# Kernel optimization log

Measured on AMD Instinct MI355X. Metric: run time of the kernel, lower is better.

The kernel has to match this reference:

```python
import jax, jax.numpy as jnp
import numpy as np

N, M, K = 8192, 100000, 4096


def setup_inputs() -> dict:
    key = jax.random.key(0)
    k0, k1, k2, k3, k4, k5 = jax.random.split(key, 6)
    origins = jax.random.uniform(k0, (N, 2), dtype=jnp.float32)
    directions = jax.random.uniform(k1, (N, 2), dtype=jnp.float32)
    embeddings = jax.random.uniform(k2, (M, 4), dtype=jnp.float32)
    # Cholesky factors: lower-triangular with strictly positive diagonal
    # (mirrors Encoder.update_parameters: tril + abs(diag)+eps)
    L = jnp.tril(jax.random.uniform(k3, (M, 4, 4), dtype=jnp.float32) * 0.1)
    i4 = jnp.arange(4)
    diag = jnp.abs(L[:, i4, i4]) + 1e-2
    chol = L.at[:, i4, i4].set(diag)
    # labels_embedding in {-1, +1} (Encoder maps 0 -> -1)
    labels = jnp.where(jax.random.randint(k4, (M,), 0, 2) == 0, -1.0, 1.0).astype(jnp.float32)
    idx = jax.random.randint(k5, (K,), 0, M, dtype=jnp.int32)
    return {"origins": origins, "directions": directions, "embeddings": embeddings,
            "chol": chol, "labels": labels, "idx": idx}


def reference(origins, directions, embeddings, chol, labels, idx):
    # Encoder: gather selected gaussians, Sigma = L @ L^T
    mu = embeddings[idx]                                   # [K,4]
    Lsel = chol[idx]                                       # [K,4,4]
    Sigma = jnp.einsum('kij,klj->kil', Lsel, Lsel)         # [K,4,4]
    lab = labels[idx]                                      # [K]
    # Decoder: batched 4x4 inverse + quadratic form + exp + sum + sigmoid
    Sigma_inv = jnp.linalg.inv(Sigma)                      # [K,4,4]
    pos = jnp.concatenate([origins, directions], axis=1)   # [N,4]
    diffs = pos[:, None, :] - mu[None, :, :]               # [N,K,4]
    q = jnp.einsum('nkd,kde,nke->nk', diffs, Sigma_inv, diffs)  # [N,K]
    pdf = lab[None, :] * jnp.exp(-0.5 * q)                 # [N,K]
    prob = jax.nn.sigmoid(jnp.sum(pdf, axis=1))            # [N]
    return prob.reshape(-1, 1)
```

## Files before the change

### kernel.cpp

```cpp
#include <hip/hip_runtime.h>
#include <math.h>

#define K_TOTAL 4096
#define N_RAYS  8192
#define S_CHUNKS 128
#define CHUNK (K_TOTAL / S_CHUNKS)
#define R 4
#define BLOCK 256
#define RAYS_PER_BLOCK (BLOCK * R)
#define NGROUPS (N_RAYS / RAYS_PER_BLOCK)

__global__ __launch_bounds__(256) void precompute_kernel(
    const float* __restrict__ embeddings,
    const float* __restrict__ chol,
    const float* __restrict__ labels,
    const int*   __restrict__ idx,
    float4*      __restrict__ tab)
{
    int k = blockIdx.x * blockDim.x + threadIdx.x;
    if (k >= K_TOTAL) return;
    int i = idx[k];

    const float* Lp = chol + (size_t)i * 16;
    float l00 = Lp[0];
    float l10 = Lp[4],  l11 = Lp[5];
    float l20 = Lp[8],  l21 = Lp[9],  l22 = Lp[10];
    float l30 = Lp[12], l31 = Lp[13], l32 = Lp[14], l33 = Lp[15];

    float u0 = 1.0f / l00, u1 = 1.0f / l11, u2 = 1.0f / l22, u3 = 1.0f / l33;

    float m00 = u0;
    float m10 = -u1 * (l10 * m00);
    float m11 = u1;
    float m20 = -u2 * (l20 * m00 + l21 * m10);
    float m21 = -u2 * (l21 * m11);
    float m22 = u2;
    float m30 = -u3 * (l30 * m00 + l31 * m10 + l32 * m20);
    float m31 = -u3 * (l31 * m11 + l32 * m21);
    float m32 = -u3 * (l32 * m22);
    float m33 = u3;

    const float SC = 0.84932180381996511548f;
    m00 *= SC; m10 *= SC; m11 *= SC; m20 *= SC; m21 *= SC;
    m22 *= SC; m30 *= SC; m31 *= SC; m32 *= SC; m33 *= SC;

    float4 mu = *(const float4*)(embeddings + (size_t)i * 4);
    float b0 = -(m00 * mu.x);
    float b1 = -(m10 * mu.x + m11 * mu.y);
    float b2 = -(m20 * mu.x + m21 * mu.y + m22 * mu.z);
    float b3 = -(m30 * mu.x + m31 * mu.y + m32 * mu.z + m33 * mu.w);

    float lab = labels[i];

    tab[4*k + 0] = make_float4(m00, m10, m11, m20);
    tab[4*k + 1] = make_float4(m21, m22, m30, m31);
    tab[4*k + 2] = make_float4(m32, m33, b0, b1);
    tab[4*k + 3] = make_float4(b2, b3, lab, 0.0f);
}

__global__ __launch_bounds__(256) void main_kernel(
    const float*  __restrict__ origins,
    const float*  __restrict__ directions,
    const float4* __restrict__ tab,
    float*        __restrict__ partial)
{
    int tid  = threadIdx.x;
    int base = blockIdx.x * RAYS_PER_BLOCK + tid;
    int s    = blockIdx.y;

    float p0[R], p1[R], p2[R], p3[R], acc[R];
    #pragma unroll
    for (int r = 0; r < R; ++r) {
        int n = base + r * BLOCK;
        float2 o = ((const float2*)origins)[n];
        float2 d = ((const float2*)directions)[n];
        p0[r] = o.x; p1[r] = o.y; p2[r] = d.x; p3[r] = d.y;
        acc[r] = 0.0f;
    }

    const float4* __restrict__ t = tab + (size_t)s * CHUNK * 4;

    #pragma unroll 4
    for (int k = 0; k < CHUNK; ++k) {
        float4 t0 = t[4*k + 0];
        float4 t1 = t[4*k + 1];
        float4 t2 = t[4*k + 2];
        float4 t3 = t[4*k + 3];
        #pragma unroll
        for (int r = 0; r < R; ++r) {
            float y0 = fmaf(t0.x, p0[r], t2.z);
            float y1 = fmaf(t0.z, p1[r], fmaf(t0.y, p0[r], t2.w));
            float y2 = fmaf(t1.y, p2[r], fmaf(t1.x, p1[r], fmaf(t0.w, p0[r], t3.x)));
            float y3 = fmaf(t2.y, p3[r], fmaf(t2.x, p2[r], fmaf(t1.w, p1[r], fmaf(t1.z, p0[r], t3.y))));
            float sq = y0 * y0;
            sq = fmaf(y1, y1, sq);
            sq = fmaf(y2, y2, sq);
            sq = fmaf(y3, y3, sq);
            acc[r] = fmaf(t3.z, __builtin_amdgcn_exp2f(-sq), acc[r]);
        }
    }

    #pragma unroll
    for (int r = 0; r < R; ++r)
        partial[(size_t)s * N_RAYS + base + r * BLOCK] = acc[r];
}

__global__ __launch_bounds__(256) void finish_kernel(
    const float* __restrict__ partial,
    float*       __restrict__ out)
{
    int n = blockIdx.x * 256 + threadIdx.x;
    float sum = 0.0f;
    #pragma unroll 8
    for (int s = 0; s < S_CHUNKS; ++s)
        sum += partial[(size_t)s * N_RAYS + n];
    const float L2E = 1.44269504088896340736f;
    out[n] = 1.0f / (1.0f + __builtin_amdgcn_exp2f(-sum * L2E));
}

extern "C" void kernel_launch(void* const* d_in, const int* in_sizes, int n_in,
                              void* d_out, int out_size, void* d_ws, size_t ws_size,
                              hipStream_t stream) {
    const float* origins    = (const float*)d_in[0];
    const float* directions = (const float*)d_in[1];
    const float* embeddings = (const float*)d_in[2];
    const float* chol       = (const float*)d_in[3];
    const float* labels     = (const float*)d_in[4];
    const int*   idx        = (const int*)d_in[5];
    float* out = (float*)d_out;

    float4* tab     = (float4*)d_ws;
    float*  partial = (float*)((char*)d_ws + (size_t)K_TOTAL * 4 * sizeof(float4));

    precompute_kernel<<<dim3(K_TOTAL / 256), dim3(256), 0, stream>>>(
        embeddings, chol, labels, idx, tab);

    main_kernel<<<dim3(NGROUPS, S_CHUNKS), dim3(256), 0, stream>>>(
        origins, directions, tab, partial);

    finish_kernel<<<dim3(N_RAYS / 256), dim3(256), 0, stream>>>(partial, out);
}
```

Baseline: 93.19 us.

## Fuse Gaussian precompute into main kernel via shared-memory table

Removes the separate precompute kernel launch. Each block of the main kernel now computes the 32-entry scaled inverse-Cholesky table for its chunk into shared memory, then reads parameters from LDS instead of global memory. Each chunk's table is recomputed by all 8 ray-group blocks, and a __syncthreads is added. The finish kernel is retuned to 64-thread blocks with a deeper unroll, and the main loop unroll is raised to 8.

```diff
diff --git a/kernel.cpp b/kernel.cpp
--- a/kernel.cpp
+++ b/kernel.cpp
@@ -10,63 +10,62 @@
 #define RAYS_PER_BLOCK (BLOCK * R)
 #define NGROUPS (N_RAYS / RAYS_PER_BLOCK)
 
-__global__ __launch_bounds__(256) void precompute_kernel(
+__global__ __launch_bounds__(256) void fused_main_kernel(
+    const float* __restrict__ origins,
+    const float* __restrict__ directions,
     const float* __restrict__ embeddings,
     const float* __restrict__ chol,
     const float* __restrict__ labels,
     const int*   __restrict__ idx,
-    float4*      __restrict__ tab)
+    float*       __restrict__ partial)
 {
-    int k = blockIdx.x * blockDim.x + threadIdx.x;
-    if (k >= K_TOTAL) return;
-    int i = idx[k];
+    __shared__ float4 stab[CHUNK * 4];
 
-    const float* Lp = chol + (size_t)i * 16;
-    float l00 = Lp[0];
-    float l10 = Lp[4],  l11 = Lp[5];
-    float l20 = Lp[8],  l21 = Lp[9],  l22 = Lp[10];
-    float l30 = Lp[12], l31 = Lp[13], l32 = Lp[14], l33 = Lp[15];
+    int tid = threadIdx.x;
+    int s   = blockIdx.y;
 
-    float u0 = 1.0f / l00, u1 = 1.0f / l11, u2 = 1.0f / l22, u3 = 1.0f / l33;
+    if (tid < CHUNK) {
+        int k = s * CHUNK + tid;
+        int i = idx[k];
 
-    float m00 = u0;
-    float m10 = -u1 * (l10 * m00);
-    float m11 = u1;
-    float m20 = -u2 * (l20 * m00 + l21 * m10);
-    float m21 = -u2 * (l21 * m11);
-    float m22 = u2;
-    float m30 = -u3 * (l30 * m00 + l31 * m10 + l32 * m20);
-    float m31 = -u3 * (l31 * m11 + l32 * m21);
-    float m32 = -u3 * (l32 * m22);
-    float m33 = u3;
+        const float* Lp = chol + (size_t)i * 16;
+        float l00 = Lp[0];
+        float l10 = Lp[4],  l11 = Lp[5];
+        float l20 = Lp[8],  l21 = Lp[9],  l22 = Lp[10];
+        float l30 = Lp[12], l31 = Lp[13], l32 = Lp[14], l33 = Lp[15];
 
-    const float SC = 0.84932180381996511548f;
-    m00 *= SC; m10 *= SC; m11 *= SC; m20 *= SC; m21 *= SC;
-    m22 *= SC; m30 *= SC; m31 *= SC; m32 *= SC; m33 *= SC;
+        float u0 = 1.0f / l00, u1 = 1.0f / l11, u2 = 1.0f / l22, u3 = 1.0f / l33;
 
-    float4 mu = *(const float4*)(embeddings + (size_t)i * 4);
-    float b0 = -(m00 * mu.x);
-    float b1 = -(m10 * mu.x + m11 * mu.y);
-    float b2 = -(m20 * mu.x + m21 * mu.y + m22 * mu.z);
-    float b3 = -(m30 * mu.x + m31 * mu.y + m32 * mu.z + m33 * mu.w);
+        float m00 = u0;
+        float m10 = -u1 * (l10 * m00);
+        float m11 = u1;
+        float m20 = -u2 * (l20 * m00 + l21 * m10);
+        float m21 = -u2 * (l21 * m11);
+        float m22 = u2;
+        float m30 = -u3 * (l30 * m00 + l31 * m10 + l32 * m20);
+        float m31 = -u3 * (l31 * m11 + l32 * m21);
+        float m32 = -u3 * (l32 * m22);
+        float m33 = u3;
 
-    float lab = labels[i];
+        const float SC = 0.84932180381996511548f;
+        m00 *= SC; m10 *= SC; m11 *= SC; m20 *= SC; m21 *= SC;
+        m22 *= SC; m30 *= SC; m31 *= SC; m32 *= SC; m33 *= SC;
 
-    tab[4*k + 0] = make_float4(m00, m10, m11, m20);
-    tab[4*k + 1] = make_float4(m21, m22, m30, m31);
-    tab[4*k + 2] = make_float4(m32, m33, b0, b1);
-    tab[4*k + 3] = make_float4(b2, b3, lab, 0.0f);
-}
+        float4 mu = *(const float4*)(embeddings + (size_t)i * 4);
+        float b0 = -(m00 * mu.x);
+        float b1 = -(m10 * mu.x + m11 * mu.y);
+        float b2 = -(m20 * mu.x + m21 * mu.y + m22 * mu.z);
+        float b3 = -(m30 * mu.x + m31 * mu.y + m32 * mu.z + m33 * mu.w);
 
-__global__ __launch_bounds__(256) void main_kernel(
-    const float*  __restrict__ origins,
-    const float*  __restrict__ directions,
-    const float4* __restrict__ tab,
-    float*        __restrict__ partial)
-{
-    int tid  = threadIdx.x;
+        float lab = labels[i];
+
+        stab[tid*4 + 0] = make_float4(m00, m10, m11, m20);
+        stab[tid*4 + 1] = make_float4(m21, m22, m30, m31);
+        stab[tid*4 + 2] = make_float4(m32, m33, b0, b1);
+        stab[tid*4 + 3] = make_float4(b2, b3, lab, 0.0f);
+    }
+
     int base = blockIdx.x * RAYS_PER_BLOCK + tid;
-    int s    = blockIdx.y;
 
     float p0[R], p1[R], p2[R], p3[R], acc[R];
     #pragma unroll
@@ -78,14 +77,14 @@
         acc[r] = 0.0f;
     }
 
-    const float4* __restrict__ t = tab + (size_t)s * CHUNK * 4;
+    __syncthreads();
 
-    #pragma unroll 4
+    #pragma unroll 8
     for (int k = 0; k < CHUNK; ++k) {
-        float4 t0 = t[4*k + 0];
-        float4 t1 = t[4*k + 1];
-        float4 t2 = t[4*k + 2];
-        float4 t3 = t[4*k + 3];
+        float4 t0 = stab[k*4 + 0];
+        float4 t1 = stab[k*4 + 1];
+        float4 t2 = stab[k*4 + 2];
+        float4 t3 = stab[k*4 + 3];
         #pragma unroll
         for (int r = 0; r < R; ++r) {
             float y0 = fmaf(t0.x, p0[r], t2.z);
@@ -105,13 +104,13 @@
         partial[(size_t)s * N_RAYS + base + r * BLOCK] = acc[r];
 }
 
-__global__ __launch_bounds__(256) void finish_kernel(
+__global__ __launch_bounds__(64) void finish_kernel(
     const float* __restrict__ partial,
     float*       __restrict__ out)
 {
-    int n = blockIdx.x * 256 + threadIdx.x;
+    int n = blockIdx.x * 64 + threadIdx.x;
     float sum = 0.0f;
-    #pragma unroll 8
+    #pragma unroll 16
     for (int s = 0; s < S_CHUNKS; ++s)
         sum += partial[(size_t)s * N_RAYS + n];
     const float L2E = 1.44269504088896340736f;
@@ -129,14 +128,10 @@
     const int*   idx        = (const int*)d_in[5];
     float* out = (float*)d_out;
 
-    float4* tab     = (float4*)d_ws;
-    float*  partial = (float*)((char*)d_ws + (size_t)K_TOTAL * 4 * sizeof(float4));
+    float* partial = (float*)d_ws;
 
-    precompute_kernel<<<dim3(K_TOTAL / 256), dim3(256), 0, stream>>>(
-        embeddings, chol, labels, idx, tab);
+    fused_main_kernel<<<dim3(NGROUPS, S_CHUNKS), dim3(BLOCK), 0, stream>>>(
+        origins, directions, embeddings, chol, labels, idx, partial);
 
-    main_kernel<<<dim3(NGROUPS, S_CHUNKS), dim3(256), 0, stream>>>(
-        origins, directions, tab, partial);
-
-    finish_kernel<<<dim3(N_RAYS / 256), dim3(256), 0, stream>>>(partial, out);
+    finish_kernel<<<dim3(N_RAYS / 64), dim3(64), 0, stream>>>(partial, out);
 }
```

Result: faster. 89.00 us (-4.5%).
